# Kernel optimization log

Hardware: AMD Instinct MI355X
Metric: run time of the kernel (lower is better)

The kernel has to match this reference:

```python
import jax, jax.numpy as jnp
import numpy as np
from jax import lax

N_PTS = 256          # hardcoded point count in original loops
BIG = 257.0 ** 2     # initial SE sentinel in original code


def setup_inputs() -> dict:
    key = jax.random.key(0)
    k1, k2 = jax.random.split(key)
    B = 2048
    inp = jax.random.normal(k1, (B, 1, 2 * N_PTS), dtype=jnp.float32)
    tgt = jax.random.normal(k2, (B, 1, 2 * N_PTS), dtype=jnp.float32)
    return {"input": inp, "targets": tgt}


def reference(input, targets):
    B = input.shape[0]
    # interleaved (x, y) pairs -> [B, 256, 2]
    pin = input[:, 0, :].reshape(B, N_PTS, 2)
    ptg = targets[:, 0, :].reshape(B, N_PTS, 2)
    # pairwise squared distances: D[b, j, k] = ||tgt_j - in_k||^2
    D = jnp.sum((ptg[:, :, None, :] - pin[:, None, :, :]) ** 2, axis=-1)  # [B,256,256]
    big = jnp.asarray(BIG, dtype=D.dtype)
    batch_idx = jnp.arange(B)

    def step(used, dj):
        # dj: [B, 256] distances from target point j to all input points
        vals = jnp.where(used, jnp.inf, dj)
        m = jnp.min(vals, axis=1)
        k = jnp.argmin(vals, axis=1)
        se = jnp.minimum(m, big)              # SE stays 257^2 if nothing beats it
        k = jnp.where(m < big, k, 0)          # k_tmp stays 0 in that case
        used = used.at[batch_idx, k].set(True)
        return used, se

    used0 = jnp.zeros((B, N_PTS), dtype=bool)
    _, ses = lax.scan(step, used0, jnp.swapaxes(D, 0, 1))  # iterate j=0..255, ses: [256, B]
    loss = jnp.sum(ses) / B / (2 * N_PTS)
    return loss
```

## Files before the change

kernel.cpp:

```cpp
#include <hip/hip_runtime.h>
#include <stdint.h>

#define N_PTS 256

typedef unsigned long long ull;
typedef float v2f __attribute__((ext_vector_type(2)));

template<int CTRL>
__device__ __forceinline__ int dppmov(int x) {
    return __builtin_amdgcn_update_dpp(0, x, CTRL, 0xF, 0xF, true);
}

__device__ __forceinline__ double rowmin16(double x) {
    #define STAGE(C) { \
        ull u = __double_as_longlong(x); \
        int lo = dppmov<C>((int)(unsigned)u); \
        int hi = dppmov<C>((int)(unsigned)(u >> 32)); \
        double r = __longlong_as_double(((ull)(unsigned)hi << 32) | (unsigned)lo); \
        x = fmin(x, r); }
    STAGE(0x121)
    STAGE(0x122)
    STAGE(0x124)
    STAGE(0x128)
    #undef STAGE
    return x;
}

__device__ __forceinline__ void reduce16(const float (&d)[16], unsigned used,
                                         unsigned rl16, unsigned& kk, unsigned& mu) {
    double kd[16];
    #pragma unroll
    for (int s = 0; s < 16; ++s) {
        unsigned du = __float_as_uint(d[s]);
        unsigned lo = (du << 8) | (unsigned)(s << 4) | rl16;
        unsigned hi = (du >> 24) | (((used >> s) & 1u) << 7);
        kd[s] = __longlong_as_double(((ull)hi << 32) | lo);
    }
    #pragma unroll
    for (int s = 0; s < 8; ++s) kd[s] = fmin(kd[s], kd[s + 8]);
    #pragma unroll
    for (int s = 0; s < 4; ++s) kd[s] = fmin(kd[s], kd[s + 4]);
    kd[0] = fmin(kd[0], kd[2]);
    kd[1] = fmin(kd[1], kd[3]);
    double km = rowmin16(fmin(kd[0], kd[1]));
    ull u = __double_as_longlong(km);
    unsigned lo = (unsigned)u, hi = (unsigned)(u >> 32);
    kk = lo & 0xFFu;
    mu = (lo >> 8) | (hi << 24);
}

__device__ __forceinline__ void finalize(unsigned kk, unsigned mu,
                                         unsigned& k, float& se) {
    const unsigned BIG_U = 0x47810200u;
    k  = (mu < BIG_U) ? kk : 0u;
    se = __uint_as_float(mu < BIG_U ? mu : BIG_U);
}

__device__ __forceinline__ void claim(unsigned sk, unsigned rl16, unsigned& used) {
    unsigned sbit = 1u << (sk >> 4);
    used |= (rl16 == (sk & 15u)) ? sbit : 0u;
}

__global__ __launch_bounds__(256, 2) void greedy_match_kernel(
    const float* __restrict__ input,
    const float* __restrict__ targets,
    float* __restrict__ out,
    int B, float scale)
{
    __shared__ v2f   tl[4][N_PTS];
    __shared__ float wsum[4];

    const unsigned lane = threadIdx.x & 63;
    const int      wid  = threadIdx.x >> 6;
    const int      b    = blockIdx.x * 4 + wid;
    const bool     vB   = (b < B);
    const int      cb   = vB ? b : 0;

    const unsigned rl16 = lane & 15u;
    const unsigned rowv = lane >> 4;

    const v2f* pin = (const v2f*)(input   + (size_t)cb * (2 * N_PTS));
    const v2f* ptg = (const v2f*)(targets + (size_t)cb * (2 * N_PTS));

    #pragma unroll
    for (int c = 0; c < 4; ++c) {
        int idx = c * 64 + (int)lane;
        tl[wid][idx] = ptg[idx];
    }
    __syncthreads();
    const v2f* tlw = tl[wid];

    v2f p[16];
    #pragma unroll
    for (int s = 0; s < 16; ++s) p[s] = pin[(s << 4) + rl16];

    unsigned used = 0u;
    float acc = 0.0f;

    {
        #pragma clang fp contract(off)
        v2f tcur = tlw[rowv];

        #pragma unroll 1
        for (int g = 0; g < 64; ++g) {
            v2f tnext = tlw[(((g + 1) & 63) << 2) + rowv];

            float d[16];
            #pragma unroll
            for (int s = 0; s < 16; ++s) {
                v2f q = tcur - p[s];
                v2f qq = q * q;
                d[s] = qq.x + qq.y;
            }

            unsigned kk, mu, kf; float sef;
            reduce16(d, used, rl16, kk, mu);
            finalize(kk, mu, kf, sef);
            unsigned vk = kf; float vse = sef;

            unsigned k0 = (unsigned)__builtin_amdgcn_readlane((int)vk, 0);
            unsigned k1 = (unsigned)__builtin_amdgcn_readlane((int)vk, 16);
            unsigned k2 = (unsigned)__builtin_amdgcn_readlane((int)vk, 32);
            unsigned k3 = (unsigned)__builtin_amdgcn_readlane((int)vk, 48);

            claim(k0, rl16, used);
            if (k1 == k0) {
                reduce16(d, used, rl16, kk, mu); finalize(kk, mu, kf, sef);
                bool upd = (rowv >= 1u);
                vk = upd ? kf : vk; vse = upd ? sef : vse;
                k1 = (unsigned)__builtin_amdgcn_readlane((int)vk, 16);
                k2 = (unsigned)__builtin_amdgcn_readlane((int)vk, 32);
                k3 = (unsigned)__builtin_amdgcn_readlane((int)vk, 48);
            }
            claim(k1, rl16, used);
            if (k2 == k0 || k2 == k1) {
                reduce16(d, used, rl16, kk, mu); finalize(kk, mu, kf, sef);
                bool upd = (rowv >= 2u);
                vk = upd ? kf : vk; vse = upd ? sef : vse;
                k2 = (unsigned)__builtin_amdgcn_readlane((int)vk, 32);
                k3 = (unsigned)__builtin_amdgcn_readlane((int)vk, 48);
            }
            claim(k2, rl16, used);
            if (k3 == k0 || k3 == k1 || k3 == k2) {
                reduce16(d, used, rl16, kk, mu); finalize(kk, mu, kf, sef);
                bool upd = (rowv >= 3u);
                vk = upd ? kf : vk; vse = upd ? sef : vse;
                k3 = (unsigned)__builtin_amdgcn_readlane((int)vk, 48);
            }
            claim(k3, rl16, used);

            acc += vse;
            tcur = tnext;
        }
    }

    int t1 = __builtin_amdgcn_ds_swizzle(__float_as_int(acc), 0x401F);
    float a2 = acc + __int_as_float(t1);
    int t2 = __builtin_amdgcn_ds_bpermute((int)((lane ^ 32u) << 2), __float_as_int(a2));
    float tot = a2 + __int_as_float(t2);

    if (lane == 0) wsum[wid] = vB ? tot : 0.0f;
    __syncthreads();
    if (threadIdx.x == 0) {
        float s = (wsum[0] + wsum[1] + wsum[2] + wsum[3]) * scale;
        atomicAdd(out, s);
    }
}

extern "C" void kernel_launch(void* const* d_in, const int* in_sizes, int n_in,
                              void* d_out, int out_size, void* d_ws, size_t ws_size,
                              hipStream_t stream) {
    const float* input   = (const float*)d_in[0];
    const float* targets = (const float*)d_in[1];
    float* out = (float*)d_out;

    const int B = in_sizes[0] / (2 * N_PTS);
    const float scale = 1.0f / ((float)B * (float)(2 * N_PTS));

    hipMemsetAsync(d_out, 0, sizeof(float) * (size_t)out_size, stream);

    const int blocks = (B + 3) / 4;
    greedy_match_kernel<<<blocks, 256, 0, stream>>>(input, targets, out, B, scale);
}
```

Before: 116.0 us.

## Software-pipeline distance computation and simplify packed min-key encoding

The loop is unrolled by two with ping-pong distance buffers, so distances for the next target row are computed while the current row's reduction and readlane chain run. This is meant to hide the latency of that serial chain. The packed 64-bit key now puts a subtracted distance and the used flag in the high word and a precomputed inverted index in the low word, and reduces with fmax. That cuts the shift and or work per element. In exchange it holds 16 more live floats and 16 precomputed index words, which could hurt occupancy under the two-waves launch bound.

```diff
diff --git a/kernel.cpp b/kernel.cpp
--- a/kernel.cpp
+++ b/kernel.cpp
@@ -11,13 +11,13 @@
     return __builtin_amdgcn_update_dpp(0, x, CTRL, 0xF, 0xF, true);
 }
 
-__device__ __forceinline__ double rowmin16(double x) {
+__device__ __forceinline__ double rowmax16(double x) {
     #define STAGE(C) { \
         ull u = __double_as_longlong(x); \
         int lo = dppmov<C>((int)(unsigned)u); \
         int hi = dppmov<C>((int)(unsigned)(u >> 32)); \
         double r = __longlong_as_double(((ull)(unsigned)hi << 32) | (unsigned)lo); \
-        x = fmin(x, r); }
+        x = fmax(x, r); }
     STAGE(0x121)
     STAGE(0x122)
     STAGE(0x124)
@@ -27,26 +27,27 @@
 }
 
 __device__ __forceinline__ void reduce16(const float (&d)[16], unsigned used,
-                                         unsigned rl16, unsigned& kk, unsigned& mu) {
+                                         const unsigned (&lc)[16],
+                                         unsigned& kk, unsigned& mu) {
+    const unsigned SGN = 0x80000000u, KH = 0x7F000000u;
     double kd[16];
     #pragma unroll
     for (int s = 0; s < 16; ++s) {
         unsigned du = __float_as_uint(d[s]);
-        unsigned lo = (du << 8) | (unsigned)(s << 4) | rl16;
-        unsigned hi = (du >> 24) | (((used >> s) & 1u) << 7);
-        kd[s] = __longlong_as_double(((ull)hi << 32) | lo);
+        unsigned t  = used << (31 - s);
+        unsigned hi = (t & SGN) | (KH - du);
+        kd[s] = __longlong_as_double(((ull)hi << 32) | lc[s]);
     }
     #pragma unroll
-    for (int s = 0; s < 8; ++s) kd[s] = fmin(kd[s], kd[s + 8]);
+    for (int s = 0; s < 8; ++s) kd[s] = fmax(kd[s], kd[s + 8]);
     #pragma unroll
-    for (int s = 0; s < 4; ++s) kd[s] = fmin(kd[s], kd[s + 4]);
-    kd[0] = fmin(kd[0], kd[2]);
-    kd[1] = fmin(kd[1], kd[3]);
-    double km = rowmin16(fmin(kd[0], kd[1]));
+    for (int s = 0; s < 4; ++s) kd[s] = fmax(kd[s], kd[s + 4]);
+    kd[0] = fmax(kd[0], kd[2]);
+    kd[1] = fmax(kd[1], kd[3]);
+    double km = rowmax16(fmax(kd[0], kd[1]));
     ull u = __double_as_longlong(km);
-    unsigned lo = (unsigned)u, hi = (unsigned)(u >> 32);
-    kk = lo & 0xFFu;
-    mu = (lo >> 8) | (hi << 24);
+    kk = 255u - (unsigned)u;
+    mu = KH - (unsigned)(u >> 32);
 }
 
 __device__ __forceinline__ void finalize(unsigned kk, unsigned mu,
@@ -91,67 +92,77 @@
     const v2f* tlw = tl[wid];
 
     v2f p[16];
+    unsigned lc[16];
     #pragma unroll
-    for (int s = 0; s < 16; ++s) p[s] = pin[(s << 4) + rl16];
+    for (int s = 0; s < 16; ++s) {
+        p[s]  = pin[(s << 4) + rl16];
+        lc[s] = 255u - (unsigned)((s << 4) | rl16);
+    }
 
     unsigned used = 0u;
     float acc = 0.0f;
 
     {
         #pragma clang fp contract(off)
-        v2f tcur = tlw[rowv];
+
+        float dA[16], dB[16];
+        {
+            v2f t0 = tlw[rowv];
+            #pragma unroll
+            for (int s = 0; s < 16; ++s) {
+                v2f q = t0 - p[s]; v2f qq = q * q; dA[s] = qq.x + qq.y;
+            }
+        }
+
+        #define STEP(dcur, dnext, g)                                          \
+        {                                                                     \
+            unsigned kk, mu, kf; float sef;                                   \
+            reduce16(dcur, used, lc, kk, mu);                                 \
+            finalize(kk, mu, kf, sef);                                        \
+            unsigned vk = kf; float vse = sef;                                \
+            v2f tn = tlw[((((g) + 1) & 63) << 2) + rowv];                     \
+            _Pragma("unroll")                                                 \
+            for (int s = 0; s < 16; ++s) {                                    \
+                v2f q = tn - p[s]; v2f qq = q * q; (dnext)[s] = qq.x + qq.y;  \
+            }                                                                 \
+            unsigned k0 = (unsigned)__builtin_amdgcn_readlane((int)vk, 0);    \
+            unsigned k1 = (unsigned)__builtin_amdgcn_readlane((int)vk, 16);   \
+            unsigned k2 = (unsigned)__builtin_amdgcn_readlane((int)vk, 32);   \
+            unsigned k3 = (unsigned)__builtin_amdgcn_readlane((int)vk, 48);   \
+            claim(k0, rl16, used);                                            \
+            if (k1 == k0) {                                                   \
+                reduce16(dcur, used, lc, kk, mu); finalize(kk, mu, kf, sef);  \
+                bool upd = (rowv >= 1u);                                      \
+                vk = upd ? kf : vk; vse = upd ? sef : vse;                    \
+                k1 = (unsigned)__builtin_amdgcn_readlane((int)vk, 16);        \
+                k2 = (unsigned)__builtin_amdgcn_readlane((int)vk, 32);        \
+                k3 = (unsigned)__builtin_amdgcn_readlane((int)vk, 48);        \
+            }                                                                 \
+            claim(k1, rl16, used);                                            \
+            if (k2 == k0 || k2 == k1) {                                       \
+                reduce16(dcur, used, lc, kk, mu); finalize(kk, mu, kf, sef);  \
+                bool upd = (rowv >= 2u);                                      \
+                vk = upd ? kf : vk; vse = upd ? sef : vse;                    \
+                k2 = (unsigned)__builtin_amdgcn_readlane((int)vk, 32);        \
+                k3 = (unsigned)__builtin_amdgcn_readlane((int)vk, 48);        \
+            }                                                                 \
+            claim(k2, rl16, used);                                            \
+            if (k3 == k0 || k3 == k1 || k3 == k2) {                           \
+                reduce16(dcur, used, lc, kk, mu); finalize(kk, mu, kf, sef);  \
+                bool upd = (rowv >= 3u);                                      \
+                vk = upd ? kf : vk; vse = upd ? sef : vse;                    \
+                k3 = (unsigned)__builtin_amdgcn_readlane((int)vk, 48);        \
+            }                                                                 \
+            claim(k3, rl16, used);                                            \
+            acc += vse;                                                      \
+        }
 
         #pragma unroll 1
-        for (int g = 0; g < 64; ++g) {
-            v2f tnext = tlw[(((g + 1) & 63) << 2) + rowv];
-
-            float d[16];
-            #pragma unroll
-            for (int s = 0; s < 16; ++s) {
-                v2f q = tcur - p[s];
-                v2f qq = q * q;
-                d[s] = qq.x + qq.y;
-            }
-
-            unsigned kk, mu, kf; float sef;
-            reduce16(d, used, rl16, kk, mu);
-            finalize(kk, mu, kf, sef);
-            unsigned vk = kf; float vse = sef;
-
-            unsigned k0 = (unsigned)__builtin_amdgcn_readlane((int)vk, 0);
-            unsigned k1 = (unsigned)__builtin_amdgcn_readlane((int)vk, 16);
-            unsigned k2 = (unsigned)__builtin_amdgcn_readlane((int)vk, 32);
-            unsigned k3 = (unsigned)__builtin_amdgcn_readlane((int)vk, 48);
-
-            claim(k0, rl16, used);
-            if (k1 == k0) {
-                reduce16(d, used, rl16, kk, mu); finalize(kk, mu, kf, sef);
-                bool upd = (rowv >= 1u);
-                vk = upd ? kf : vk; vse = upd ? sef : vse;
-                k1 = (unsigned)__builtin_amdgcn_readlane((int)vk, 16);
-                k2 = (unsigned)__builtin_amdgcn_readlane((int)vk, 32);
-                k3 = (unsigned)__builtin_amdgcn_readlane((int)vk, 48);
-            }
-            claim(k1, rl16, used);
-            if (k2 == k0 || k2 == k1) {
-                reduce16(d, used, rl16, kk, mu); finalize(kk, mu, kf, sef);
-                bool upd = (rowv >= 2u);
-                vk = upd ? kf : vk; vse = upd ? sef : vse;
-                k2 = (unsigned)__builtin_amdgcn_readlane((int)vk, 32);
-                k3 = (unsigned)__builtin_amdgcn_readlane((int)vk, 48);
-            }
-            claim(k2, rl16, used);
-            if (k3 == k0 || k3 == k1 || k3 == k2) {
-                reduce16(d, used, rl16, kk, mu); finalize(kk, mu, kf, sef);
-                bool upd = (rowv >= 3u);
-                vk = upd ? kf : vk; vse = upd ? sef : vse;
-                k3 = (unsigned)__builtin_amdgcn_readlane((int)vk, 48);
-            }
-            claim(k3, rl16, used);
-
-            acc += vse;
-            tcur = tnext;
+        for (int g = 0; g < 64; g += 2) {
+            STEP(dA, dB, g)
+            STEP(dB, dA, g + 1)
         }
+        #undef STEP
     }
 
     int t1 = __builtin_amdgcn_ds_swizzle(__float_as_int(acc), 0x401F);
@@ -177,7 +188,7 @@
     const int B = in_sizes[0] / (2 * N_PTS);
     const float scale = 1.0f / ((float)B * (float)(2 * N_PTS));
 
-    hipMemsetAsync(d_out, 0, sizeof(float) * (size_t)out_size, stream);
+    (void)hipMemsetAsync(d_out, 0, sizeof(float) * (size_t)out_size, stream);
 
     const int blocks = (B + 3) / 4;
     greedy_match_kernel<<<blocks, 256, 0, stream>>>(input, targets, out, B, scale);
```

New measurement: 109.5 us. 1.06x faster.
